# Kernel optimization log

Hardware: AMD Instinct MI355X
Metric: run time of the kernel (lower is better)

The kernel has to match this reference:

```python
import jax, jax.numpy as jnp
import numpy as np

N_NODES = 50000
N_EDGES = 800000
HIDDEN = 128
IN_DIM = 128
OUT_DIM = 1
N_LAYERS = 4
N_GRAPHS = 32
LN_EPS = 1e-5


def setup_inputs() -> dict:
    key = jax.random.key(0)
    ks = jax.random.split(key, 12)
    s = 1.0 / np.sqrt(HIDDEN)
    inp = {
        "x": jax.random.normal(ks[0], (N_NODES, IN_DIM), dtype=jnp.float32),
        "edge_index": jax.random.randint(ks[1], (2, N_EDGES), 0, N_NODES, dtype=jnp.int64),
        "batch": jnp.sort(jax.random.randint(ks[2], (N_NODES,), 0, N_GRAPHS, dtype=jnp.int64)),
        "W_emb": jax.random.normal(ks[3], (HIDDEN, IN_DIM), dtype=jnp.float32) * s,
        "b_emb": jax.random.normal(ks[4], (HIDDEN,), dtype=jnp.float32) * s,
        "W_layers": jax.random.normal(ks[5], (N_LAYERS, HIDDEN, HIDDEN), dtype=jnp.float32) * s,
        "b_layers": jax.random.normal(ks[6], (N_LAYERS, HIDDEN), dtype=jnp.float32) * s,
        "ln_gamma": 1.0 + 0.02 * jax.random.normal(ks[7], (N_LAYERS, HIDDEN), dtype=jnp.float32),
        "ln_beta": 0.02 * jax.random.normal(ks[8], (N_LAYERS, HIDDEN), dtype=jnp.float32),
        "W_out": jax.random.normal(ks[9], (OUT_DIM, HIDDEN), dtype=jnp.float32) * s,
    }
    return inp


def _layer_norm(x, gamma, beta):
    mu = jnp.mean(x, axis=-1, keepdims=True)
    var = jnp.mean(jnp.square(x - mu), axis=-1, keepdims=True)
    return (x - mu) * jax.lax.rsqrt(var + LN_EPS) * gamma + beta


def reference(x, edge_index, batch, W_emb, b_emb, W_layers, b_layers, ln_gamma, ln_beta, W_out):
    n = x.shape[0]
    # add self-loops (PyG GCNConv default)
    loop = jnp.arange(n, dtype=edge_index.dtype)
    row = jnp.concatenate([edge_index[0], loop])  # source nodes
    col = jnp.concatenate([edge_index[1], loop])  # target nodes
    # symmetric normalization: deg over targets
    deg = jax.ops.segment_sum(jnp.ones_like(col, dtype=x.dtype), col, num_segments=n)
    dis = jnp.where(deg > 0, jax.lax.rsqrt(jnp.maximum(deg, 1.0)), 0.0)
    norm = dis[row] * dis[col]  # [E+N]

    h = x @ W_emb.T + b_emb  # embedding layer
    for i in range(N_LAYERS):
        t = h @ W_layers[i].T                      # [N, H] linear first
        msg = t[row] * norm[:, None]               # gather + scale  [E+N, H]
        agg = jax.ops.segment_sum(msg, col, num_segments=n) + b_layers[i]
        h = _layer_norm(h + jax.nn.relu(agg), ln_gamma[i], ln_beta[i])

    out = h @ W_out.T                              # [N, OUT_DIM]
    sums = jax.ops.segment_sum(out, batch, num_segments=N_GRAPHS)
    cnts = jax.ops.segment_sum(jnp.ones((n,), out.dtype), batch, num_segments=N_GRAPHS)
    return sums / jnp.maximum(cnts, 1.0)[:, None]  # [N_GRAPHS, OUT_DIM]
```

## Files before the change

kernel.cpp:

```cpp
#include <hip/hip_runtime.h>
#include <hip/hip_fp16.h>

#define NN 50000
#define NE 800000
#define NETOT (NE + NN)
#define NH 128
#define NG 32
#define NL 4
#define NB 196
#define EMBB 782
#define HISTB 3125
#define PREP4B 256
#define NTILE 12500
#define WSLOT (NH * NH)

typedef __attribute__((ext_vector_type(8))) short bf16x8;
typedef __attribute__((ext_vector_type(4))) float f32x4;
typedef __attribute__((ext_vector_type(2))) float f32x2;

__device__ inline short f2bf(float x) {
  union { float f; unsigned u; } v;
  v.f = x;
  unsigned r = v.u + 0x7FFF + ((v.u >> 16) & 1);
  return (short)(r >> 16);
}
__device__ inline float bf2f(short s) {
  union { unsigned u; float f; } v;
  v.u = ((unsigned)(unsigned short)s) << 16;
  return v.f;
}

__device__ inline int pdw(int t, int quad) {
  return (((2 * t + (quad >> 1)) & 3) << 3) + ((t >> 1) << 1) + (quad & 1);
}

__device__ inline void fp8row_fma(float (&ag)[4][8], uint4 qa, uint4 qb,
                                  float w) {
  const unsigned dw[8] = {qa.x, qa.y, qa.z, qa.w, qb.x, qb.y, qb.z, qb.w};
#pragma unroll
  for (int ks = 0; ks < 4; ++ks) {
    f32x2 u0 = __builtin_amdgcn_cvt_pk_f32_fp8(dw[2 * ks], 0);
    f32x2 u1 = __builtin_amdgcn_cvt_pk_f32_fp8(dw[2 * ks], 1);
    f32x2 u2 = __builtin_amdgcn_cvt_pk_f32_fp8(dw[2 * ks + 1], 0);
    f32x2 u3 = __builtin_amdgcn_cvt_pk_f32_fp8(dw[2 * ks + 1], 1);
    ag[ks][0] += u0.x * w; ag[ks][1] += u0.y * w;
    ag[ks][2] += u1.x * w; ag[ks][3] += u1.y * w;
    ag[ks][4] += u2.x * w; ag[ks][5] += u2.y * w;
    ag[ks][6] += u3.x * w; ag[ks][7] += u3.y * w;
  }
}

__device__ inline int block_exscan(int v) {
  __shared__ int wsum[4];
  int tid = threadIdx.x, wave = tid >> 6, lane = tid & 63;
  int x = v;
#pragma unroll
  for (int off = 1; off < 64; off <<= 1) {
    int y = __shfl_up(x, off, 64);
    if (lane >= off) x += y;
  }
  if (lane == 63) wsum[wave] = x;
  __syncthreads();
  int wp = 0;
  if (wave > 0) wp += wsum[0];
  if (wave > 1) wp += wsum[1];
  if (wave > 2) wp += wsum[2];
  return wp + x - v;
}

__global__ __launch_bounds__(256) void prep_hist_emb_kernel(
    const float* __restrict__ Xf, const float* __restrict__ W_emb,
    const float* __restrict__ W_layers, short* __restrict__ hi,
    short* __restrict__ lo, const int* __restrict__ row,
    const int* __restrict__ col, int* __restrict__ cnt4, int* __restrict__ rank,
    const float* __restrict__ bias, __half* __restrict__ hnew,
    unsigned char* __restrict__ h8) {
  __shared__ short Wh[WSLOT];
  __shared__ short Wl[WSLOT];
  int tid = threadIdx.x;
  int blk = blockIdx.x;
  if (blk >= EMBB) {
    if (blk < EMBB + HISTB) {
      int e = (blk - EMBB) * 256 + tid;
      if (e < NE) {
        int s = row[e];
        int t = s / NTILE;
        rank[e] = atomicAdd(&cnt4[col[e] * 4 + t], 1);
      }
    } else {
      int i = (blk - EMBB - HISTB) * 256 + tid;
      if (i < 4 * WSLOT) {
        int slot = i >> 14, f = i & (WSLOT - 1);
        int j = f & 7, lane = (f >> 3) & 63, tt = (f >> 9) & 7, ks = f >> 12;
        int n = tt * 16 + (lane & 15);
        int k = ks * 32 + ((lane >> 4) & 3) * 8 + j;
        const float* W = W_layers + (size_t)slot * WSLOT;
        float x = W[n * NH + k];
        short hh = f2bf(x);
        hi[i] = hh;
        lo[i] = f2bf(x - bf2f(hh));
      }
    }
    return;
  }

#pragma unroll
  for (int i = tid * 8; i < WSLOT; i += 256 * 8) {
    int f = i;
    int lane8 = (f >> 3) & 63, tt = (f >> 9) & 7, ks = f >> 12;
    int n = tt * 16 + (lane8 & 15);
    int k0 = ks * 32 + ((lane8 >> 4) & 3) * 8;
    const float* wr = W_emb + n * NH + k0;
    float4 a0 = *(const float4*)wr;
    float4 a1 = *(const float4*)(wr + 4);
    float wv[8] = {a0.x, a0.y, a0.z, a0.w, a1.x, a1.y, a1.z, a1.w};
    bf16x8 vh, vl;
#pragma unroll
    for (int j = 0; j < 8; ++j) {
      short hh = f2bf(wv[j]);
      vh[j] = hh;
      vl[j] = f2bf(wv[j] - bf2f(hh));
    }
    *(bf16x8*)&Wh[i] = vh;
    *(bf16x8*)&Wl[i] = vl;
  }
  __syncthreads();

  int wave = tid >> 6, lane = tid & 63;
  int quad = lane >> 4, r16 = lane & 15;
  int m0 = blk * 64 + wave * 16;
  if (m0 >= NN) return;
  int mA = m0 + r16;

  f32x4 acc[8];
#pragma unroll
  for (int t = 0; t < 8; ++t) acc[t] = (f32x4){0.f, 0.f, 0.f, 0.f};

#pragma unroll
  for (int ks = 0; ks < 4; ++ks) {
    int klane = ks * 32 + quad * 8;
    const float* xr = Xf + (size_t)mA * NH + klane;
    float4 a0 = *(const float4*)xr;
    float4 a1 = *(const float4*)(xr + 4);
    float af[8] = {a0.x, a0.y, a0.z, a0.w, a1.x, a1.y, a1.z, a1.w};
    bf16x8 xhi, xlo;
#pragma unroll
    for (int j = 0; j < 8; ++j) {
      short h = f2bf(af[j]);
      xhi[j] = h;
      xlo[j] = f2bf(af[j] - bf2f(h));
    }
#pragma unroll
    for (int t = 0; t < 8; ++t) {
      int fidx = ((ks * 8 + t) * 64 + lane) << 3;
      bf16x8 whi = *(const bf16x8*)&Wh[fidx];
      bf16x8 wlo = *(const bf16x8*)&Wl[fidx];
      acc[t] = __builtin_amdgcn_mfma_f32_16x16x32_bf16(whi, xhi, acc[t], 0, 0, 0);
      acc[t] = __builtin_amdgcn_mfma_f32_16x16x32_bf16(whi, xlo, acc[t], 0, 0, 0);
      acc[t] = __builtin_amdgcn_mfma_f32_16x16x32_bf16(wlo, xhi, acc[t], 0, 0, 0);
    }
  }

  int m = m0 + r16;
  int cb = quad * 4;
#pragma unroll
  for (int t = 0; t < 8; ++t) {
    int ch = t * 16 + cb;
    float4 bb = *(const float4*)(bias + ch);
    float o0 = acc[t][0] + bb.x, o1 = acc[t][1] + bb.y;
    float o2 = acc[t][2] + bb.z, o3 = acc[t][3] + bb.w;
    __half2 p01 = __float22half2_rn(make_float2(o0, o1));
    __half2 p23 = __float22half2_rn(make_float2(o2, o3));
    *(uint2*)(hnew + (size_t)m * NH + ch) =
        make_uint2(*(unsigned*)&p01, *(unsigned*)&p23);
    int v = 0;
    v = __builtin_amdgcn_cvt_pk_fp8_f32(o0, o1, v, 0);
    v = __builtin_amdgcn_cvt_pk_fp8_f32(o2, o3, v, 1);
    ((unsigned*)(h8 + (size_t)m * NH))[pdw(t, quad)] = (unsigned)v;
  }
}

__global__ __launch_bounds__(256) void scan1_kernel(const int* __restrict__ cnt4,
                                                    int* __restrict__ bsum,
                                                    float* __restrict__ dis,
                                                    int* __restrict__ deg) {
  int i = blockIdx.x * 256 + threadIdx.x;
  int v = 0;
  if (i < NN) {
    int4 c4 = *(const int4*)&cnt4[i * 4];
    v = c4.x + c4.y + c4.z + c4.w + 1;
    deg[i] = v;
    dis[i] = rsqrtf((float)v);
  }
  int lane = threadIdx.x & 63;
  int s = v;
#pragma unroll
  for (int off = 32; off; off >>= 1) s += __shfl_down(s, off, 64);
  __shared__ int ws[4];
  if (lane == 0) ws[threadIdx.x >> 6] = s;
  __syncthreads();
  if (threadIdx.x == 0) bsum[blockIdx.x] = ws[0] + ws[1] + ws[2] + ws[3];
}

__global__ __launch_bounds__(256) void scan3b_kernel(const int* __restrict__ deg,
                                                     const int* __restrict__ bsum,
                                                     const float* __restrict__ dis,
                                                     int* __restrict__ offs,
                                                     int2* __restrict__ csr) {
  __shared__ int ws2[4];
  int tid = threadIdx.x;
  int b = blockIdx.x;
  int v = (tid < NB && tid < b) ? bsum[tid] : 0;
  int lane = tid & 63;
  int s = v;
#pragma unroll
  for (int off = 32; off; off >>= 1) s += __shfl_down(s, off, 64);
  if (lane == 0) ws2[tid >> 6] = s;
  __syncthreads();
  int bo = ws2[0] + ws2[1] + ws2[2] + ws2[3];
  int i = b * 256 + tid;
  int c = (i < NN) ? deg[i] : 0;
  int ex = block_exscan(c);
  if (i < NN) {
    int o = bo + ex;
    offs[i] = o;
    float dii = dis[i];
    csr[o + c - 1] =
        make_int2((i << 6) | (i & 63), __float_as_int(dii * dii));
  }
}

__global__ __launch_bounds__(256) void fill_kernel(const int* __restrict__ row,
                                                   const int* __restrict__ col,
                                                   const int* __restrict__ rank,
                                                   const int* __restrict__ cnt4,
                                                   const float* __restrict__ dis,
                                                   const int* __restrict__ offs,
                                                   int2* __restrict__ csr) {
  int e = blockIdx.x * 256 + threadIdx.x;
  if (e < NE) {
    int d = col[e];
    int s = row[e];
    int t = s / NTILE;
    int4 c4 = *(const int4*)&cnt4[d * 4];
    int pre = (t > 0 ? c4.x : 0) + (t > 1 ? c4.y : 0) + (t > 2 ? c4.z : 0);
    int pos = offs[d] + pre + rank[e];
    csr[pos] =
        make_int2((s << 6) | (d & 63), __float_as_int(dis[s] * dis[d]));
  }
}

template <bool LAST>
__global__ __launch_bounds__(512) void layer_fused(
    const unsigned char* __restrict__ h8in, const short* __restrict__ Whi,
    const short* __restrict__ Wlo, const float* __restrict__ bias,
    const __half* __restrict__ hprev, const float* __restrict__ gamma,
    const float* __restrict__ beta, const float* __restrict__ Wout,
    const int* __restrict__ offs, const int2* __restrict__ csr,
    __half* __restrict__ hnew, unsigned char* __restrict__ h8out,
    float* __restrict__ nodeval) {
  __shared__ short Wh[WSLOT];
  __shared__ short Wl[WSLOT];
  int tid = threadIdx.x;
#pragma unroll
  for (int i = tid * 8; i < WSLOT; i += 512 * 8) {
    *(bf16x8*)&Wh[i] = *(const bf16x8*)(Whi + i);
    *(bf16x8*)&Wl[i] = *(const bf16x8*)(Wlo + i);
  }

  int wave = tid >> 6, lane = tid & 63;
  int quad = lane >> 4, r16 = lane & 15;
  int m0 = blockIdx.x * 128 + wave * 16;
  bool active = m0 < NN;
  int nd = active ? m0 + r16 : 0;
  int cb = quad * 4;

  uint2 hp[8];
#pragma unroll
  for (int t = 0; t < 8; ++t)
    hp[t] = *(const uint2*)(hprev + (size_t)nd * NH + t * 16 + cb);

  float ag[4][8];
#pragma unroll
  for (int ks = 0; ks < 4; ++ks)
#pragma unroll
    for (int j = 0; j < 8; ++j) ag[ks][j] = 0.f;

  const char* rbase = (const char*)h8in + quad * 32;
  int s0 = offs[nd];
  int e1 = active ? ((nd + 1 < NN) ? offs[nd + 1] : NETOT) : s0;
  int j = s0;
  for (; j + 2 <= e1; j += 2) {
    int2 p0 = csr[j], p1 = csr[j + 1];
    const uint4* r0 = (const uint4*)(rbase + (size_t)(((unsigned)p0.x) >> 6) * NH);
    const uint4* r1 = (const uint4*)(rbase + (size_t)(((unsigned)p1.x) >> 6) * NH);
    uint4 a0 = r0[0], b0 = r0[1];
    uint4 a1 = r1[0], b1 = r1[1];
    fp8row_fma(ag, a0, b0, __int_as_float(p0.y));
    fp8row_fma(ag, a1, b1, __int_as_float(p1.y));
  }
  if (j < e1) {
    int2 p0 = csr[j];
    const uint4* r0 = (const uint4*)(rbase + (size_t)(((unsigned)p0.x) >> 6) * NH);
    uint4 a0 = r0[0], b0 = r0[1];
    fp8row_fma(ag, a0, b0, __int_as_float(p0.y));
  }

  __syncthreads();

  if (!active) return;

  f32x4 acc[8];
#pragma unroll
  for (int t = 0; t < 8; ++t) acc[t] = (f32x4){0.f, 0.f, 0.f, 0.f};

#pragma unroll
  for (int ks = 0; ks < 4; ++ks) {
    bf16x8 xhi, xlo;
#pragma unroll
    for (int q = 0; q < 8; ++q) {
      short hh = f2bf(ag[ks][q]);
      xhi[q] = hh;
      xlo[q] = f2bf(ag[ks][q] - bf2f(hh));
    }
#pragma unroll
    for (int t = 0; t < 8; ++t) {
      int fidx = ((ks * 8 + t) * 64 + lane) << 3;
      bf16x8 whi = *(const bf16x8*)&Wh[fidx];
      bf16x8 wlo = *(const bf16x8*)&Wl[fidx];
      acc[t] = __builtin_amdgcn_mfma_f32_16x16x32_bf16(whi, xhi, acc[t], 0, 0, 0);
      acc[t] = __builtin_amdgcn_mfma_f32_16x16x32_bf16(whi, xlo, acc[t], 0, 0, 0);
      acc[t] = __builtin_amdgcn_mfma_f32_16x16x32_bf16(wlo, xhi, acc[t], 0, 0, 0);
    }
  }

  int m = nd;
  float vv[8][4];
  float s = 0.f, s2 = 0.f;
#pragma unroll
  for (int t = 0; t < 8; ++t) {
    int ch = t * 16 + cb;
    float4 bb = *(const float4*)(bias + ch);
    float2 h01 = __half22float2(*(__half2*)&hp[t].x);
    float2 h23 = __half22float2(*(__half2*)&hp[t].y);
    float hv[4] = {h01.x, h01.y, h23.x, h23.y};
    float bb4[4] = {bb.x, bb.y, bb.z, bb.w};
#pragma unroll
    for (int r = 0; r < 4; ++r) {
      float z = fmaxf(acc[t][r] + bb4[r], 0.f);
      float val = hv[r] + z;
      vv[t][r] = val;
      s += val;
      s2 += val * val;
    }
  }
  s += __shfl_xor(s, 16, 64);
  s += __shfl_xor(s, 32, 64);
  s2 += __shfl_xor(s2, 16, 64);
  s2 += __shfl_xor(s2, 32, 64);
  float mean = s * (1.f / 128.f);
  float var = fmaxf(s2 * (1.f / 128.f) - mean * mean, 0.f);
  float inv = rsqrtf(var + 1e-5f);
  float d = 0.f;
#pragma unroll
  for (int t = 0; t < 8; ++t) {
    int ch = t * 16 + cb;
    float4 gv = *(const float4*)(gamma + ch);
    float4 bt = *(const float4*)(beta + ch);
    float o0 = (vv[t][0] - mean) * inv * gv.x + bt.x;
    float o1 = (vv[t][1] - mean) * inv * gv.y + bt.y;
    float o2 = (vv[t][2] - mean) * inv * gv.z + bt.z;
    float o3 = (vv[t][3] - mean) * inv * gv.w + bt.w;
    if (!LAST) {
      __half2 p01 = __float22half2_rn(make_float2(o0, o1));
      __half2 p23 = __float22half2_rn(make_float2(o2, o3));
      *(uint2*)(hnew + (size_t)m * NH + ch) =
          make_uint2(*(unsigned*)&p01, *(unsigned*)&p23);
      int pv = 0;
      pv = __builtin_amdgcn_cvt_pk_fp8_f32(o0, o1, pv, 0);
      pv = __builtin_amdgcn_cvt_pk_fp8_f32(o2, o3, pv, 1);
      ((unsigned*)(h8out + (size_t)m * NH))[pdw(t, quad)] = (unsigned)pv;
    } else {
      float4 wv = *(const float4*)(Wout + ch);
      d += o0 * wv.x + o1 * wv.y + o2 * wv.z + o3 * wv.w;
    }
  }
  if (LAST) {
    d += __shfl_xor(d, 16, 64);
    d += __shfl_xor(d, 32, 64);
    if (lane < 16) nodeval[m] = d;
  }
}

__global__ __launch_bounds__(256) void reduce_pool_kernel(
    const float* __restrict__ nodeval, const int* __restrict__ batch,
    float* __restrict__ gsum, int* __restrict__ gcnt, int* __restrict__ done,
    float* __restrict__ out) {
  __shared__ float bins[NG];
  __shared__ int cbins[NG];
  __shared__ int lastflag;
  int tid = threadIdx.x;
  if (tid < NG) {
    bins[tid] = 0.f;
    cbins[tid] = 0;
  }
  __syncthreads();
  int i = blockIdx.x * 256 + tid;
  if (i < NN) {
    int g = batch[i];
    atomicAdd(&bins[g], nodeval[i]);
    atomicAdd(&cbins[g], 1);
  }
  __syncthreads();
  if (tid < NG && cbins[tid]) {
    atomicAdd(&gsum[tid], bins[tid]);
    atomicAdd(&gcnt[tid], cbins[tid]);
  }
  __threadfence();
  if (tid == 0) lastflag = (atomicAdd(done, 1) == (int)gridDim.x - 1);
  __syncthreads();
  if (lastflag && tid < NG) {
    float sv = atomicAdd(&gsum[tid], 0.f);
    int cv = atomicAdd(&gcnt[tid], 0);
    out[tid] = sv / fmaxf((float)cv, 1.0f);
  }
}

extern "C" void kernel_launch(void* const* d_in, const int* in_sizes, int n_in,
                              void* d_out, int out_size, void* d_ws, size_t ws_size,
                              hipStream_t stream) {
  const float* x = (const float*)d_in[0];
  const int* eidx = (const int*)d_in[1];
  const int* batch = (const int*)d_in[2];
  const float* W_emb = (const float*)d_in[3];
  const float* b_emb = (const float*)d_in[4];
  const float* W_layers = (const float*)d_in[5];
  const float* b_layers = (const float*)d_in[6];
  const float* ln_gamma = (const float*)d_in[7];
  const float* ln_beta = (const float*)d_in[8];
  const float* W_out = (const float*)d_in[9];
  float* out = (float*)d_out;

  char* ws = (char*)d_ws;
  unsigned char* h8a = (unsigned char*)ws; ws += (size_t)NN * NH;
  unsigned char* h8b = (unsigned char*)ws; ws += (size_t)NN * NH;
  __half* h = (__half*)ws;      ws += (size_t)NN * NH * 2;
  short* Whi = (short*)ws;      ws += (size_t)4 * WSLOT * 2;
  short* Wlo = (short*)ws;      ws += (size_t)4 * WSLOT * 2;
  float* dis = (float*)ws;      ws += (size_t)NN * 4;
  int2* csr = (int2*)ws;        ws += (size_t)NETOT * 8;
  int* rank = (int*)ws;         ws += (size_t)NE * 4;
  int* offs = (int*)ws;         ws += (size_t)NN * 4;
  int* deg = (int*)ws;          ws += (size_t)NN * 4;
  float* nodeval = (float*)ws;  ws += (size_t)NN * 4;
  int* bsum = (int*)ws;         ws += (size_t)NB * 4;
  char* zero_base = ws;
  int* cnt4 = (int*)ws;         ws += (size_t)NN * 16;
  float* gsum = (float*)ws;     ws += (size_t)NG * 4;
  int* gcnt = (int*)ws;         ws += (size_t)NG * 4;
  int* done = (int*)ws;         ws += 64;
  size_t zero_bytes = (size_t)(ws - zero_base);
  hipMemsetAsync(zero_base, 0, zero_bytes, stream);

  const int* erow = eidx;
  const int* ecol = eidx + NE;

  prep_hist_emb_kernel<<<EMBB + HISTB + PREP4B, 256, 0, stream>>>(
      x, W_emb, W_layers, Whi, Wlo, erow, ecol, cnt4, rank, b_emb, h, h8a);
  scan1_kernel<<<NB, 256, 0, stream>>>(cnt4, bsum, dis, deg);
  scan3b_kernel<<<NB, 256, 0, stream>>>(deg, bsum, dis, offs, csr);
  fill_kernel<<<HISTB, 256, 0, stream>>>(erow, ecol, rank, cnt4, dis, offs, csr);

  int gblk = (NN + 127) / 128;
  for (int l = 0; l < NL; ++l) {
    const short* wh = Whi + (size_t)l * WSLOT;
    const short* wl = Wlo + (size_t)l * WSLOT;
    const float* bl = b_layers + (size_t)l * NH;
    const float* gl = ln_gamma + (size_t)l * NH;
    const float* be = ln_beta + (size_t)l * NH;
    const unsigned char* hin = (l & 1) ? h8b : h8a;
    unsigned char* hout = (l & 1) ? h8a : h8b;
    if (l == NL - 1)
      layer_fused<true><<<gblk, 512, 0, stream>>>(
          hin, wh, wl, bl, h, gl, be, W_out, offs, csr, h, nullptr, nodeval);
    else
      layer_fused<false><<<gblk, 512, 0, stream>>>(
          hin, wh, wl, bl, h, gl, be, nullptr, offs, csr, h, hout, nullptr);
  }
  reduce_pool_kernel<<<NB, 256, 0, stream>>>(nodeval, batch, gsum, gcnt, done,
                                             out);
}
```

Measured before the change: 331.2 us.

## Degree-bucket node permutation for balanced gathers and fuse graph pooling into last layer

Adds a counting sort of nodes by clamped in-degree (histogram in scan1, bucket placement in scan3b) and has each layer process nodes in that permuted order. The 16 nodes a wave handles then have similar edge counts, which cuts the idle lanes in the per-row gather loop. Per-graph node counts are now computed early, and the mean-pooling reduction moves into the last layer kernel, which removes the separate reduce kernel and the nodeval buffer. The cost is scattered per-node reads and writes of h, since nodes are no longer contiguous within a block, plus a small amount of extra atomic work.

```diff
diff --git a/kernel.cpp b/kernel.cpp
--- a/kernel.cpp
+++ b/kernel.cpp
@@ -180,34 +180,46 @@
   }
 }
 
-__global__ __launch_bounds__(256) void scan1_kernel(const int* __restrict__ cnt4,
-                                                    int* __restrict__ bsum,
-                                                    float* __restrict__ dis,
-                                                    int* __restrict__ deg) {
-  int i = blockIdx.x * 256 + threadIdx.x;
+__global__ __launch_bounds__(256) void scan1_kernel(
+    const int* __restrict__ cnt4, int* __restrict__ bsum,
+    float* __restrict__ dis, int* __restrict__ deg,
+    const int* __restrict__ batch, int* __restrict__ gcnt,
+    int* __restrict__ dhist) {
+  __shared__ int gbins[NG];
+  __shared__ int dbins[64];
+  __shared__ int ws[4];
+  int tid = threadIdx.x;
+  if (tid < NG) gbins[tid] = 0;
+  if (tid < 64) dbins[tid] = 0;
+  __syncthreads();
+  int i = blockIdx.x * 256 + tid;
   int v = 0;
   if (i < NN) {
     int4 c4 = *(const int4*)&cnt4[i * 4];
     v = c4.x + c4.y + c4.z + c4.w + 1;
     deg[i] = v;
     dis[i] = rsqrtf((float)v);
-  }
-  int lane = threadIdx.x & 63;
+    atomicAdd(&gbins[batch[i]], 1);
+    atomicAdd(&dbins[min(v, 63)], 1);
+  }
+  int lane = tid & 63;
   int s = v;
 #pragma unroll
   for (int off = 32; off; off >>= 1) s += __shfl_down(s, off, 64);
-  __shared__ int ws[4];
-  if (lane == 0) ws[threadIdx.x >> 6] = s;
-  __syncthreads();
-  if (threadIdx.x == 0) bsum[blockIdx.x] = ws[0] + ws[1] + ws[2] + ws[3];
-}
-
-__global__ __launch_bounds__(256) void scan3b_kernel(const int* __restrict__ deg,
-                                                     const int* __restrict__ bsum,
-                                                     const float* __restrict__ dis,
-                                                     int* __restrict__ offs,
-                                                     int2* __restrict__ csr) {
+  if (lane == 0) ws[tid >> 6] = s;
+  __syncthreads();
+  if (tid == 0) bsum[blockIdx.x] = ws[0] + ws[1] + ws[2] + ws[3];
+  if (tid < NG && gbins[tid]) atomicAdd(&gcnt[tid], gbins[tid]);
+  if (tid < 64 && dbins[tid]) atomicAdd(&dhist[tid], dbins[tid]);
+}
+
+__global__ __launch_bounds__(256) void scan3b_kernel(
+    const int* __restrict__ deg, const int* __restrict__ bsum,
+    const float* __restrict__ dis, int* __restrict__ offs,
+    int2* __restrict__ csr, const int* __restrict__ dhist,
+    int* __restrict__ dcnt, int* __restrict__ perm) {
   __shared__ int ws2[4];
+  __shared__ int pbase_s[64];
   int tid = threadIdx.x;
   int b = blockIdx.x;
   int v = (tid < NB && tid < b) ? bsum[tid] : 0;
@@ -227,6 +239,22 @@
     float dii = dis[i];
     csr[o + c - 1] =
         make_int2((i << 6) | (i & 63), __float_as_int(dii * dii));
+  }
+  if (tid < 64) {
+    int x = dhist[tid];
+    int incl = x;
+#pragma unroll
+    for (int off = 1; off < 64; off <<= 1) {
+      int y = __shfl_up(incl, off, 64);
+      if (tid >= off) incl += y;
+    }
+    pbase_s[tid] = incl - x;
+  }
+  __syncthreads();
+  if (i < NN) {
+    int bin = min(c, 63);
+    int r = atomicAdd(&dcnt[bin], 1);
+    perm[pbase_s[bin] + r] = i;
   }
 }
 
@@ -257,10 +285,14 @@
     const __half* __restrict__ hprev, const float* __restrict__ gamma,
     const float* __restrict__ beta, const float* __restrict__ Wout,
     const int* __restrict__ offs, const int2* __restrict__ csr,
-    __half* __restrict__ hnew, unsigned char* __restrict__ h8out,
-    float* __restrict__ nodeval) {
+    const int* __restrict__ perm, __half* __restrict__ hnew,
+    unsigned char* __restrict__ h8out, const int* __restrict__ batch,
+    float* __restrict__ gsum, const int* __restrict__ gcnt,
+    int* __restrict__ done, float* __restrict__ out) {
   __shared__ short Wh[WSLOT];
   __shared__ short Wl[WSLOT];
+  __shared__ int2 pool_s[128];
+  __shared__ int lastflag_s;
   int tid = threadIdx.x;
 #pragma unroll
   for (int i = tid * 8; i < WSLOT; i += 512 * 8) {
@@ -272,7 +304,7 @@
   int quad = lane >> 4, r16 = lane & 15;
   int m0 = blockIdx.x * 128 + wave * 16;
   bool active = m0 < NN;
-  int nd = active ? m0 + r16 : 0;
+  int nd = active ? perm[m0 + r16] : 0;
   int cb = quad * 4;
 
   uint2 hp[8];
@@ -308,121 +340,117 @@
 
   __syncthreads();
 
-  if (!active) return;
-
-  f32x4 acc[8];
-#pragma unroll
-  for (int t = 0; t < 8; ++t) acc[t] = (f32x4){0.f, 0.f, 0.f, 0.f};
-
-#pragma unroll
-  for (int ks = 0; ks < 4; ++ks) {
-    bf16x8 xhi, xlo;
-#pragma unroll
-    for (int q = 0; q < 8; ++q) {
-      short hh = f2bf(ag[ks][q]);
-      xhi[q] = hh;
-      xlo[q] = f2bf(ag[ks][q] - bf2f(hh));
-    }
+  if (!LAST) {
+    if (!active) return;
+  }
+
+  float dval = 0.f;
+  int gnd = 0;
+  if (active) {
+    f32x4 acc[8];
+#pragma unroll
+    for (int t = 0; t < 8; ++t) acc[t] = (f32x4){0.f, 0.f, 0.f, 0.f};
+
+#pragma unroll
+    for (int ks = 0; ks < 4; ++ks) {
+      bf16x8 xhi, xlo;
+#pragma unroll
+      for (int q = 0; q < 8; ++q) {
+        short hh = f2bf(ag[ks][q]);
+        xhi[q] = hh;
+        xlo[q] = f2bf(ag[ks][q] - bf2f(hh));
+      }
+#pragma unroll
+      for (int t = 0; t < 8; ++t) {
+        int fidx = ((ks * 8 + t) * 64 + lane) << 3;
+        bf16x8 whi = *(const bf16x8*)&Wh[fidx];
+        bf16x8 wlo = *(const bf16x8*)&Wl[fidx];
+        acc[t] = __builtin_amdgcn_mfma_f32_16x16x32_bf16(whi, xhi, acc[t], 0, 0, 0);
+        acc[t] = __builtin_amdgcn_mfma_f32_16x16x32_bf16(whi, xlo, acc[t], 0, 0, 0);
+        acc[t] = __builtin_amdgcn_mfma_f32_16x16x32_bf16(wlo, xhi, acc[t], 0, 0, 0);
+      }
+    }
+
+    int m = nd;
+    float vv[8][4];
+    float s = 0.f, s2 = 0.f;
 #pragma unroll
     for (int t = 0; t < 8; ++t) {
-      int fidx = ((ks * 8 + t) * 64 + lane) << 3;
-      bf16x8 whi = *(const bf16x8*)&Wh[fidx];
-      bf16x8 wlo = *(const bf16x8*)&Wl[fidx];
-      acc[t] = __builtin_amdgcn_mfma_f32_16x16x32_bf16(whi, xhi, acc[t], 0, 0, 0);
-      acc[t] = __builtin_amdgcn_mfma_f32_16x16x32_bf16(whi, xlo, acc[t], 0, 0, 0);
-      acc[t] = __builtin_amdgcn_mfma_f32_16x16x32_bf16(wlo, xhi, acc[t], 0, 0, 0);
-    }
-  }
-
-  int m = nd;
-  float vv[8][4];
-  float s = 0.f, s2 = 0.f;
-#pragma unroll
-  for (int t = 0; t < 8; ++t) {
-    int ch = t * 16 + cb;
-    float4 bb = *(const float4*)(bias + ch);
-    float2 h01 = __half22float2(*(__half2*)&hp[t].x);
-    float2 h23 = __half22float2(*(__half2*)&hp[t].y);
-    float hv[4] = {h01.x, h01.y, h23.x, h23.y};
-    float bb4[4] = {bb.x, bb.y, bb.z, bb.w};
-#pragma unroll
-    for (int r = 0; r < 4; ++r) {
-      float z = fmaxf(acc[t][r] + bb4[r], 0.f);
-      float val = hv[r] + z;
-      vv[t][r] = val;
-      s += val;
-      s2 += val * val;
-    }
-  }
-  s += __shfl_xor(s, 16, 64);
-  s += __shfl_xor(s, 32, 64);
-  s2 += __shfl_xor(s2, 16, 64);
-  s2 += __shfl_xor(s2, 32, 64);
-  float mean = s * (1.f / 128.f);
-  float var = fmaxf(s2 * (1.f / 128.f) - mean * mean, 0.f);
-  float inv = rsqrtf(var + 1e-5f);
-  float d = 0.f;
-#pragma unroll
-  for (int t = 0; t < 8; ++t) {
-    int ch = t * 16 + cb;
-    float4 gv = *(const float4*)(gamma + ch);
-    float4 bt = *(const float4*)(beta + ch);
-    float o0 = (vv[t][0] - mean) * inv * gv.x + bt.x;
-    float o1 = (vv[t][1] - mean) * inv * gv.y + bt.y;
-    float o2 = (vv[t][2] - mean) * inv * gv.z + bt.z;
-    float o3 = (vv[t][3] - mean) * inv * gv.w + bt.w;
-    if (!LAST) {
-      __half2 p01 = __float22half2_rn(make_float2(o0, o1));
-      __half2 p23 = __float22half2_rn(make_float2(o2, o3));
-      *(uint2*)(hnew + (size_t)m * NH + ch) =
-          make_uint2(*(unsigned*)&p01, *(unsigned*)&p23);
-      int pv = 0;
-      pv = __builtin_amdgcn_cvt_pk_fp8_f32(o0, o1, pv, 0);
-      pv = __builtin_amdgcn_cvt_pk_fp8_f32(o2, o3, pv, 1);
-      ((unsigned*)(h8out + (size_t)m * NH))[pdw(t, quad)] = (unsigned)pv;
-    } else {
-      float4 wv = *(const float4*)(Wout + ch);
-      d += o0 * wv.x + o1 * wv.y + o2 * wv.z + o3 * wv.w;
-    }
-  }
+      int ch = t * 16 + cb;
+      float4 bb = *(const float4*)(bias + ch);
+      float2 h01 = __half22float2(*(__half2*)&hp[t].x);
+      float2 h23 = __half22float2(*(__half2*)&hp[t].y);
+      float hv[4] = {h01.x, h01.y, h23.x, h23.y};
+      float bb4[4] = {bb.x, bb.y, bb.z, bb.w};
+#pragma unroll
+      for (int r = 0; r < 4; ++r) {
+        float z = fmaxf(acc[t][r] + bb4[r], 0.f);
+        float val = hv[r] + z;
+        vv[t][r] = val;
+        s += val;
+        s2 += val * val;
+      }
+    }
+    s += __shfl_xor(s, 16, 64);
+    s += __shfl_xor(s, 32, 64);
+    s2 += __shfl_xor(s2, 16, 64);
+    s2 += __shfl_xor(s2, 32, 64);
+    float mean = s * (1.f / 128.f);
+    float var = fmaxf(s2 * (1.f / 128.f) - mean * mean, 0.f);
+    float inv = rsqrtf(var + 1e-5f);
+    float d = 0.f;
+#pragma unroll
+    for (int t = 0; t < 8; ++t) {
+      int ch = t * 16 + cb;
+      float4 gv = *(const float4*)(gamma + ch);
+      float4 bt = *(const float4*)(beta + ch);
+      float o0 = (vv[t][0] - mean) * inv * gv.x + bt.x;
+      float o1 = (vv[t][1] - mean) * inv * gv.y + bt.y;
+      float o2 = (vv[t][2] - mean) * inv * gv.z + bt.z;
+      float o3 = (vv[t][3] - mean) * inv * gv.w + bt.w;
+      if (!LAST) {
+        __half2 p01 = __float22half2_rn(make_float2(o0, o1));
+        __half2 p23 = __float22half2_rn(make_float2(o2, o3));
+        *(uint2*)(hnew + (size_t)m * NH + ch) =
+            make_uint2(*(unsigned*)&p01, *(unsigned*)&p23);
+        int pv = 0;
+        pv = __builtin_amdgcn_cvt_pk_fp8_f32(o0, o1, pv, 0);
+        pv = __builtin_amdgcn_cvt_pk_fp8_f32(o2, o3, pv, 1);
+        ((unsigned*)(h8out + (size_t)m * NH))[pdw(t, quad)] = (unsigned)pv;
+      } else {
+        float4 wv = *(const float4*)(Wout + ch);
+        d += o0 * wv.x + o1 * wv.y + o2 * wv.z + o3 * wv.w;
+      }
+    }
+    if (LAST) {
+      d += __shfl_xor(d, 16, 64);
+      d += __shfl_xor(d, 32, 64);
+      dval = d;
+      gnd = batch[m];
+    }
+  }
+
   if (LAST) {
-    d += __shfl_xor(d, 16, 64);
-    d += __shfl_xor(d, 32, 64);
-    if (lane < 16) nodeval[m] = d;
-  }
-}
-
-__global__ __launch_bounds__(256) void reduce_pool_kernel(
-    const float* __restrict__ nodeval, const int* __restrict__ batch,
-    float* __restrict__ gsum, int* __restrict__ gcnt, int* __restrict__ done,
-    float* __restrict__ out) {
-  __shared__ float bins[NG];
-  __shared__ int cbins[NG];
-  __shared__ int lastflag;
-  int tid = threadIdx.x;
-  if (tid < NG) {
-    bins[tid] = 0.f;
-    cbins[tid] = 0;
-  }
-  __syncthreads();
-  int i = blockIdx.x * 256 + tid;
-  if (i < NN) {
-    int g = batch[i];
-    atomicAdd(&bins[g], nodeval[i]);
-    atomicAdd(&cbins[g], 1);
-  }
-  __syncthreads();
-  if (tid < NG && cbins[tid]) {
-    atomicAdd(&gsum[tid], bins[tid]);
-    atomicAdd(&gcnt[tid], cbins[tid]);
-  }
-  __threadfence();
-  if (tid == 0) lastflag = (atomicAdd(done, 1) == (int)gridDim.x - 1);
-  __syncthreads();
-  if (lastflag && tid < NG) {
-    float sv = atomicAdd(&gsum[tid], 0.f);
-    int cv = atomicAdd(&gcnt[tid], 0);
-    out[tid] = sv / fmaxf((float)cv, 1.0f);
+    if (lane < 16)
+      pool_s[wave * 16 + r16] =
+          make_int2(active ? gnd : 0, __float_as_int(active ? dval : 0.f));
+    __syncthreads();
+    if (tid < 32) {
+      float acc = 0.f;
+#pragma unroll 8
+      for (int k = 0; k < 128; ++k) {
+        int2 e = pool_s[k];
+        if (e.x == tid) acc += __int_as_float(e.y);
+      }
+      atomicAdd(&gsum[tid], acc);
+    }
+    __threadfence();
+    if (tid == 0) lastflag_s = (atomicAdd(done, 1) == (int)gridDim.x - 1);
+    __syncthreads();
+    if (lastflag_s && tid < NG) {
+      float sv = atomicAdd(&gsum[tid], 0.f);
+      out[tid] = sv / fmaxf((float)gcnt[tid], 1.0f);
+    }
   }
 }
 
@@ -452,12 +480,14 @@
   int* rank = (int*)ws;         ws += (size_t)NE * 4;
   int* offs = (int*)ws;         ws += (size_t)NN * 4;
   int* deg = (int*)ws;          ws += (size_t)NN * 4;
-  float* nodeval = (float*)ws;  ws += (size_t)NN * 4;
+  int* perm = (int*)ws;         ws += (size_t)NN * 4;
   int* bsum = (int*)ws;         ws += (size_t)NB * 4;
   char* zero_base = ws;
   int* cnt4 = (int*)ws;         ws += (size_t)NN * 16;
   float* gsum = (float*)ws;     ws += (size_t)NG * 4;
   int* gcnt = (int*)ws;         ws += (size_t)NG * 4;
+  int* dhist = (int*)ws;        ws += 64 * 4;
+  int* dcnt = (int*)ws;         ws += 64 * 4;
   int* done = (int*)ws;         ws += 64;
   size_t zero_bytes = (size_t)(ws - zero_base);
   hipMemsetAsync(zero_base, 0, zero_bytes, stream);
@@ -467,8 +497,10 @@
 
   prep_hist_emb_kernel<<<EMBB + HISTB + PREP4B, 256, 0, stream>>>(
       x, W_emb, W_layers, Whi, Wlo, erow, ecol, cnt4, rank, b_emb, h, h8a);
-  scan1_kernel<<<NB, 256, 0, stream>>>(cnt4, bsum, dis, deg);
-  scan3b_kernel<<<NB, 256, 0, stream>>>(deg, bsum, dis, offs, csr);
+  scan1_kernel<<<NB, 256, 0, stream>>>(cnt4, bsum, dis, deg, batch, gcnt,
+                                       dhist);
+  scan3b_kernel<<<NB, 256, 0, stream>>>(deg, bsum, dis, offs, csr, dhist, dcnt,
+                                        perm);
   fill_kernel<<<HISTB, 256, 0, stream>>>(erow, ecol, rank, cnt4, dis, offs, csr);
 
   int gblk = (NN + 127) / 128;
@@ -482,11 +514,11 @@
     unsigned char* hout = (l & 1) ? h8a : h8b;
     if (l == NL - 1)
       layer_fused<true><<<gblk, 512, 0, stream>>>(
-          hin, wh, wl, bl, h, gl, be, W_out, offs, csr, h, nullptr, nodeval);
+          hin, wh, wl, bl, h, gl, be, W_out, offs, csr, perm, h, nullptr,
+          batch, gsum, gcnt, done, out);
     else
       layer_fused<false><<<gblk, 512, 0, stream>>>(
-          hin, wh, wl, bl, h, gl, be, nullptr, offs, csr, h, hout, nullptr);
-  }
-  reduce_pool_kernel<<<NB, 256, 0, stream>>>(nodeval, batch, gsum, gcnt, done,
-                                             out);
-}
+          hin, wh, wl, bl, h, gl, be, nullptr, offs, csr, perm, h, hout,
+          batch, gsum, gcnt, done, out);
+  }
+}
```

New measurement: 533.7 us. 1.61x slower.
